# Performance work log

Measured on AMD Instinct MI355X. Metric: run time of the kernel, lower is better.

The kernel has to match this reference:

```python
import jax, jax.numpy as jnp
import numpy as np
from functools import partial

B, T, D = 256, 196, 512
H = 4            # nhead
DH = D // H      # head dim
DFF = 2 * D      # dim_feedforward
K = 8192         # codebook size
L = 2            # num_layers
EPS = 1e-5


def setup_inputs() -> dict:
    key = jax.random.key(0)
    ks = jax.random.split(key, 8)
    s = 0.02  # weight init scale for numerical stability
    return {
        "motion": jax.random.normal(ks[0], (B, T, D), jnp.float32),
        "conv_w": jax.random.normal(ks[1], (L, D, D, 3), jnp.float32) * s,
        "conv_b": jnp.zeros((L, D), jnp.float32),
        "wqkv": jax.random.normal(ks[2], (L, D, 3 * D), jnp.float32) * s,
        "bqkv": jnp.zeros((L, 3 * D), jnp.float32),
        "wo": jax.random.normal(ks[3], (L, D, D), jnp.float32) * s,
        "bo": jnp.zeros((L, D), jnp.float32),
        "ln1_g": jnp.ones((L, D), jnp.float32),
        "ln1_b": jnp.zeros((L, D), jnp.float32),
        "ln2_g": jnp.ones((L, D), jnp.float32),
        "ln2_b": jnp.zeros((L, D), jnp.float32),
        "w1": jax.random.normal(ks[4], (L, D, DFF), jnp.float32) * s,
        "b1": jnp.zeros((L, DFF), jnp.float32),
        "w2": jax.random.normal(ks[5], (L, DFF, D), jnp.float32) * s,
        "b2": jnp.zeros((L, D), jnp.float32),
        "codebook": jax.random.normal(ks[6], (K, D), jnp.float32),
    }


def _layer_norm(x, g, b):
    mu = jnp.mean(x, axis=-1, keepdims=True)
    var = jnp.mean(jnp.square(x - mu), axis=-1, keepdims=True)
    return (x - mu) * jax.lax.rsqrt(var + EPS) * g + b


def _causal_half_downsample(x, w, b):
    # x: [B, T, D] -> [B, ceil(T/2), D]; pad left by repeating first frame (RepeatFirstElementPad1d(2))
    xc = jnp.transpose(x, (0, 2, 1))                       # [B, D, T]
    xp = jnp.concatenate([jnp.repeat(xc[:, :, :1], 2, axis=2), xc], axis=2)
    y = jax.lax.conv_general_dilated(
        xp, w, window_strides=(2,), padding='VALID',
        dimension_numbers=('NCH', 'OIH', 'NCH'))            # [B, D, T//2]
    y = y + b[None, :, None]
    y = jax.nn.gelu(y, approximate=False)                   # torch nn.GELU default = exact
    return jnp.transpose(y, (0, 2, 1))


def _encoder_layer(x, wqkv, bqkv, wo, bo, ln1_g, ln1_b, ln2_g, ln2_b, w1, b1, w2, b2):
    # Post-LN TransformerEncoderLayer with causal self-attention, ReLU FFN (dropout=eval)
    Tl = x.shape[1]
    qkv = x @ wqkv + bqkv                                    # [B, T, 3D]
    q, k, v = jnp.split(qkv, 3, axis=-1)
    q = q.reshape(x.shape[0], Tl, H, DH)
    k = k.reshape(x.shape[0], Tl, H, DH)
    v = v.reshape(x.shape[0], Tl, H, DH)
    scores = jnp.einsum('bqhd,bkhd->bhqk', q, k) / jnp.sqrt(jnp.float32(DH))
    causal = jnp.tril(jnp.ones((Tl, Tl), bool))              # col <= row allowed
    scores = jnp.where(causal[None, None], scores, jnp.float32(-1e30))
    attn = jax.nn.softmax(scores, axis=-1)
    out = jnp.einsum('bhqk,bkhd->bqhd', attn, v).reshape(x.shape[0], Tl, D)
    x = _layer_norm(x + out @ wo + bo, ln1_g, ln1_b)
    ff = jax.nn.relu(x @ w1 + b1) @ w2 + b2
    return _layer_norm(x + ff, ln2_g, ln2_b)


def _quantize(x, codebook):
    # nearest-neighbor VQ with straight-through estimator
    flat = x.reshape(-1, D)                                   # [B*Tf, D]
    d = (jnp.sum(flat * flat, axis=1, keepdims=True)
         - 2.0 * flat @ codebook.T
         + jnp.sum(codebook * codebook, axis=1)[None, :])     # [B*Tf, K]
    idx = jnp.argmin(d, axis=-1)                              # [B*Tf]
    q = codebook[idx]
    q_st = flat + jax.lax.stop_gradient(q - flat)
    return q_st.reshape(x.shape), idx.reshape(x.shape[:2])


def reference(motion, conv_w, conv_b, wqkv, bqkv, wo, bo,
              ln1_g, ln1_b, ln2_g, ln2_b, w1, b1, w2, b2, codebook):
    x = motion
    for l in range(L):  # fixed small layer loop
        x = _causal_half_downsample(x, conv_w[l], conv_b[l])
        x = _encoder_layer(x, wqkv[l], bqkv[l], wo[l], bo[l],
                           ln1_g[l], ln1_b[l], ln2_g[l], ln2_b[l],
                           w1[l], b1[l], w2[l], b2[l])
    quant, idx = _quantize(x, codebook)
    return quant, idx
```

## Files before the change

kernel.cpp:

```cpp
#include <hip/hip_runtime.h>
#include <hip/hip_bf16.h>
#include <math.h>

#define BBATCH 256
#define DMODEL 512
#define NHEAD 4
#define DHEAD 128
#define DFFN 1024
#define KCB 8192
#define VEPS 0.02f
#define NROWS 12544
#define NSPLIT 64

typedef __attribute__((ext_vector_type(8))) short short8v;
typedef __attribute__((ext_vector_type(4))) float f32x4;

__device__ __forceinline__ void tsplit3(float x, unsigned short& h,
                                        unsigned short& m, unsigned short& l) {
    unsigned u = __float_as_uint(x);
    float hf = __uint_as_float(u & 0xffff0000u);
    float r = x - hf;
    unsigned ru = __float_as_uint(r);
    float mf = __uint_as_float(ru & 0xffff0000u);
    float r2 = r - mf;
    h = (unsigned short)(u >> 16);
    m = (unsigned short)(ru >> 16);
    l = (unsigned short)(__float_as_uint(r2) >> 16);
}

__global__ __launch_bounds__(256) void k_wsplit3T(const float* __restrict__ W, int ldw,
                                                  int K, int total,
                                                  unsigned short* __restrict__ th,
                                                  unsigned short* __restrict__ tm,
                                                  unsigned short* __restrict__ tl) {
    int idx = blockIdx.x * 256 + threadIdx.x;
    if (idx >= total) return;
    int n = idx / K, k = idx - n * K;
    unsigned short h, m, l;
    tsplit3(W[(size_t)k * ldw + n], h, m, l);
    th[idx] = h; tm[idx] = m; tl[idx] = l;
}

__global__ __launch_bounds__(256) void k_wsplit3_conv(const float* __restrict__ cw,
                                                      unsigned short* __restrict__ th,
                                                      unsigned short* __restrict__ tm,
                                                      unsigned short* __restrict__ tl) {
    int idx = blockIdx.x * 256 + threadIdx.x;
    if (idx >= DMODEL * 3 * DMODEL) return;
    int dout = idx / 1536, k = idx - dout * 1536;
    int kk = k >> 9, di = k & 511;
    unsigned short h, m, l;
    tsplit3(cw[(size_t)dout * 1536 + di * 3 + kk], h, m, l);
    th[idx] = h; tm[idx] = m; tl[idx] = l;
}

template <int ACT, int CONV>
__global__ __launch_bounds__(256) void k_gemm6(const float* __restrict__ A, int lda,
                                               const unsigned short* __restrict__ B3h,
                                               const unsigned short* __restrict__ B3m,
                                               const unsigned short* __restrict__ B3l,
                                               const float* __restrict__ bias,
                                               float* __restrict__ C, int ldc,
                                               int K, int Tin, int Tout) {
    __shared__ __align__(16) unsigned short Ah[4096], Am[4096], Al[4096];
    __shared__ __align__(16) unsigned short Bh[4096], Bm[4096], Bl[4096];

    int tid = threadIdx.x;
    int lane = tid & 63, wave = tid >> 6;
    int lrow = lane & 15, lkg = lane >> 4;
    int wr = wave >> 1, wc = wave & 1;
    int wrbase = wr * 64, wcbase = wc * 64;
    int n0 = blockIdx.x * 128, m0 = blockIdx.y * 128;

    int sr[2], ss[2]; size_t abase[2], bbase[2]; int attv[2];
#pragma unroll
    for (int rd = 0; rd < 2; rd++) {
        int slot = tid + rd * 256;
        int row = slot >> 2, seg = slot & 3;
        sr[rd] = row; ss[rd] = seg;
        bbase[rd] = (size_t)(n0 + row) * K + seg * 8;
        int m = m0 + row;
        if (CONV) {
            int b = m / Tout, tt = m - b * Tout;
            abase[rd] = (size_t)b * Tin * DMODEL;
            attv[rd] = 2 * tt - 2;
        } else {
            abase[rd] = (size_t)m * lda + seg * 8;
            attv[rd] = 0;
        }
    }

    f32x4 acc[4][4];
#pragma unroll
    for (int mi = 0; mi < 4; mi++)
#pragma unroll
        for (int ni = 0; ni < 4; ni++) acc[mi][ni] = (f32x4){0.0f, 0.0f, 0.0f, 0.0f};

    for (int k0 = 0; k0 < K; k0 += 32) {
#pragma unroll
        for (int rd = 0; rd < 2; rd++) {
            int row = sr[rd], seg = ss[rd];
            int la = row * 32 + ((seg ^ ((row >> 1) & 3)) << 3);
            *(short8v*)(Bh + la) = *(const short8v*)(B3h + bbase[rd] + k0);
            *(short8v*)(Bm + la) = *(const short8v*)(B3m + bbase[rd] + k0);
            *(short8v*)(Bl + la) = *(const short8v*)(B3l + bbase[rd] + k0);
            const float* ap;
            if (CONV) {
                int f = attv[rd] + (k0 >> 9);
                if (f < 0) f = 0;
                ap = A + abase[rd] + (size_t)f * DMODEL + (k0 & 511) + seg * 8;
            } else {
                ap = A + abase[rd] + k0;
            }
            float4 v0 = *(const float4*)ap;
            float4 v1 = *(const float4*)(ap + 4);
            float vv[8] = {v0.x, v0.y, v0.z, v0.w, v1.x, v1.y, v1.z, v1.w};
            short8v hv, mv, lv;
#pragma unroll
            for (int j = 0; j < 8; j++) {
                unsigned short h, m, l;
                tsplit3(vv[j], h, m, l);
                hv[j] = (short)h; mv[j] = (short)m; lv[j] = (short)l;
            }
            *(short8v*)(Ah + la) = hv;
            *(short8v*)(Am + la) = mv;
            *(short8v*)(Al + la) = lv;
        }
        __syncthreads();

        short8v afh[4], afm[4], afl[4];
#pragma unroll
        for (int mi = 0; mi < 4; mi++) {
            int rowa = wrbase + mi * 16 + lrow;
            int off = rowa * 32 + ((lkg ^ ((rowa >> 1) & 3)) << 3);
            afh[mi] = *(const short8v*)(Ah + off);
            afm[mi] = *(const short8v*)(Am + off);
            afl[mi] = *(const short8v*)(Al + off);
        }
#pragma unroll
        for (int ni = 0; ni < 4; ni++) {
            int rowb = wcbase + ni * 16 + lrow;
            int off = rowb * 32 + ((lkg ^ ((rowb >> 1) & 3)) << 3);
            short8v bfh = *(const short8v*)(Bh + off);
            short8v bfm = *(const short8v*)(Bm + off);
            short8v bfl = *(const short8v*)(Bl + off);
#pragma unroll
            for (int mi = 0; mi < 4; mi++) {
                acc[mi][ni] = __builtin_amdgcn_mfma_f32_16x16x32_bf16(afh[mi], bfh, acc[mi][ni], 0, 0, 0);
                acc[mi][ni] = __builtin_amdgcn_mfma_f32_16x16x32_bf16(afh[mi], bfm, acc[mi][ni], 0, 0, 0);
                acc[mi][ni] = __builtin_amdgcn_mfma_f32_16x16x32_bf16(afm[mi], bfh, acc[mi][ni], 0, 0, 0);
                acc[mi][ni] = __builtin_amdgcn_mfma_f32_16x16x32_bf16(afh[mi], bfl, acc[mi][ni], 0, 0, 0);
                acc[mi][ni] = __builtin_amdgcn_mfma_f32_16x16x32_bf16(afl[mi], bfh, acc[mi][ni], 0, 0, 0);
                acc[mi][ni] = __builtin_amdgcn_mfma_f32_16x16x32_bf16(afm[mi], bfm, acc[mi][ni], 0, 0, 0);
            }
        }
        __syncthreads();
    }

    float bv[4];
#pragma unroll
    for (int ni = 0; ni < 4; ni++) bv[ni] = bias[n0 + wcbase + ni * 16 + lrow];
#pragma unroll
    for (int mi = 0; mi < 4; mi++)
#pragma unroll
        for (int ni = 0; ni < 4; ni++)
#pragma unroll
            for (int v = 0; v < 4; v++) {
                int row = m0 + wrbase + mi * 16 + lkg * 4 + v;
                int col = n0 + wcbase + ni * 16 + lrow;
                float x;
                if (ACT == 1) {
                    double dv = (double)acc[mi][ni][v] + (double)bv[ni];
                    dv = 0.5 * dv * (1.0 + erf(dv * 0.7071067811865476));
                    x = (float)dv;
                } else {
                    x = acc[mi][ni][v] + bv[ni];
                    if (ACT == 2) x = x > 0.0f ? x : 0.0f;
                }
                C[(size_t)row * ldc + col] = x;
            }
}

__global__ __launch_bounds__(256) void k_attn(const float* q,
                                              const float* __restrict__ k,
                                              const float* __restrict__ v,
                                              float* out, int T) {
    __shared__ __align__(16) float Ks[98 * 128];
    __shared__ __align__(16) float qsm[4][128];
    __shared__ float psm[4][128];
    int h = blockIdx.x, b = blockIdx.y;
    int tid = threadIdx.x;
    int lane = tid & 63;
    int wave = tid >> 6;
    size_t base = ((size_t)b * T) * DMODEL + (size_t)h * DHEAD;

    float4* Ks4 = (float4*)Ks;
    for (int it = tid; it < T * 32; it += 256) {
        int j = it >> 5, dq = it & 31;
        Ks4[j * 32 + (dq ^ (j & 7))] =
            *(const float4*)&k[base + (size_t)j * DMODEL + dq * 4];
    }
    __syncthreads();

    const float SCALE = 0.08838834764831845f;
    int niter = (T + 3) >> 2;
    for (int i0 = 0; i0 < niter; i0++) {
        int ibase = i0 * 4;
#pragma unroll
        for (int u = 0; u < 2; u++) {
            int idx = tid + u * 256;
            int r = idx >> 7, d = idx & 127;
            int grow = ibase + r;
            if (grow < T) qsm[r][d] = q[base + (size_t)grow * DMODEL + d];
        }
        __syncthreads();

        int i = ibase + wave;
        if (i < T) {
            int j1 = lane;
            int j2 = lane + 64;
            int j2c = j2 < T ? j2 : 0;
            bool a0 = (j1 <= i);
            bool a1 = (j2 <= i);
            const float4* kr1 = Ks4 + j1 * 32;
            const float4* kr2 = Ks4 + j2c * 32;
            const float4* qr = (const float4*)qsm[wave];
            int x1 = j1 & 7, x2 = j2c & 7;
            float4 s0 = {0.f, 0.f, 0.f, 0.f}, s1 = {0.f, 0.f, 0.f, 0.f};
#pragma unroll
            for (int dq = 0; dq < 32; dq++) {
                float4 qv = qr[dq];
                float4 k1 = kr1[dq ^ x1];
                float4 k2 = kr2[dq ^ x2];
                s0.x = fmaf(qv.x, k1.x, s0.x);
                s0.y = fmaf(qv.y, k1.y, s0.y);
                s0.z = fmaf(qv.z, k1.z, s0.z);
                s0.w = fmaf(qv.w, k1.w, s0.w);
                s1.x = fmaf(qv.x, k2.x, s1.x);
                s1.y = fmaf(qv.y, k2.y, s1.y);
                s1.z = fmaf(qv.z, k2.z, s1.z);
                s1.w = fmaf(qv.w, k2.w, s1.w);
            }
            float sv0 = a0 ? ((s0.x + s0.y) + (s0.z + s0.w)) * SCALE : -1e30f;
            float sv1 = a1 ? ((s1.x + s1.y) + (s1.z + s1.w)) * SCALE : -1e30f;

            float m = fmaxf(sv0, sv1);
#pragma unroll
            for (int off = 32; off > 0; off >>= 1) m = fmaxf(m, __shfl_xor(m, off, 64));
            float p0 = a0 ? expf(sv0 - m) : 0.0f;
            float p1 = a1 ? expf(sv1 - m) : 0.0f;
            float sum = p0 + p1;
#pragma unroll
            for (int off = 32; off > 0; off >>= 1) sum += __shfl_xor(sum, off, 64);
            float inv = 1.0f / sum;

            psm[wave][lane] = p0;
            psm[wave][lane + 64] = p1;

            float o0[4] = {0.f, 0.f, 0.f, 0.f}, o1[4] = {0.f, 0.f, 0.f, 0.f};
            const float* vb = v + base;
            for (int j = 0; j <= i; j += 4) {
#pragma unroll
                for (int u = 0; u < 4; u++) {
                    int jj = j + u;
                    float pj = psm[wave][jj];
                    int jr = jj < T ? jj : T - 1;
                    const float* vr = vb + (size_t)jr * DMODEL;
                    o0[u] = fmaf(pj, vr[lane], o0[u]);
                    o1[u] = fmaf(pj, vr[lane + 64], o1[u]);
                }
            }
            out[base + (size_t)i * DMODEL + lane] =
                ((o0[0] + o0[1]) + (o0[2] + o0[3])) * inv;
            out[base + (size_t)i * DMODEL + lane + 64] =
                ((o1[0] + o1[1]) + (o1[2] + o1[3])) * inv;
        }
        __syncthreads();
    }
}

__global__ __launch_bounds__(128) void k_ln(const float* __restrict__ resid,
                                            const float* __restrict__ y,
                                            const float* __restrict__ g,
                                            const float* __restrict__ bta,
                                            float* __restrict__ out) {
    int row = blockIdx.x;
    int tid = threadIdx.x;
    size_t off = (size_t)row * DMODEL;
    double t[4];
#pragma unroll
    for (int i = 0; i < 4; i++) {
        int d = tid + i * 128;
        t[i] = (double)resid[off + d] + (double)y[off + d];
    }
    __shared__ double rd[2];
    double s = t[0] + t[1] + t[2] + t[3];
#pragma unroll
    for (int o = 32; o > 0; o >>= 1) s += __shfl_down(s, o, 64);
    if ((tid & 63) == 0) rd[tid >> 6] = s;
    __syncthreads();
    double mean = (rd[0] + rd[1]) * (1.0 / 512.0);
    double vs = 0.0;
#pragma unroll
    for (int i = 0; i < 4; i++) { double dl = t[i] - mean; vs += dl * dl; }
    __syncthreads();
#pragma unroll
    for (int o = 32; o > 0; o >>= 1) vs += __shfl_down(vs, o, 64);
    if ((tid & 63) == 0) rd[tid >> 6] = vs;
    __syncthreads();
    double var = (rd[0] + rd[1]) * (1.0 / 512.0);
    double scale = 1.0 / sqrt(var + 1e-5);
#pragma unroll
    for (int i = 0; i < 4; i++) {
        int d = tid + i * 128;
        out[off + d] = (float)((t[i] - mean) * scale * (double)g[d] + (double)bta[d]);
    }
}

__global__ __launch_bounds__(64) void k_cbn(const float* __restrict__ cb,
                                            double* __restrict__ cbn) {
    int row = blockIdx.x;
    int tid = threadIdx.x;
    const float* r = cb + (size_t)row * DMODEL;
    double s = 0.0;
    for (int d = tid; d < DMODEL; d += 64) { double v = (double)r[d]; s = fma(v, v, s); }
#pragma unroll
    for (int o = 32; o > 0; o >>= 1) s += __shfl_down(s, o, 64);
    if (tid == 0) cbn[row] = s;
}

__device__ __forceinline__ unsigned short f2bf(float f) {
    unsigned u = __float_as_uint(f);
    unsigned r = (u + 0x7fffu + ((u >> 16) & 1u)) >> 16;
    return (unsigned short)r;
}
__device__ __forceinline__ float bf2f(unsigned short h) {
    return __uint_as_float(((unsigned)h) << 16);
}

__global__ __launch_bounds__(256) void k_split(const float* __restrict__ in,
                                               unsigned short* __restrict__ hi,
                                               unsigned short* __restrict__ lo,
                                               int n4) {
    int i = blockIdx.x * 256 + threadIdx.x;
    if (i >= n4) return;
    float4 v = ((const float4*)in)[i];
    float vv[4] = {v.x, v.y, v.z, v.w};
    unsigned short h[4], l[4];
#pragma unroll
    for (int j = 0; j < 4; j++) {
        h[j] = f2bf(vv[j]);
        l[j] = f2bf(vv[j] - bf2f(h[j]));
    }
    ((ushort4*)hi)[i] = make_ushort4(h[0], h[1], h[2], h[3]);
    ((ushort4*)lo)[i] = make_ushort4(l[0], l[1], l[2], l[3]);
}

__global__ __launch_bounds__(256) void k_cbT(const float* __restrict__ cb,
                                             float* __restrict__ cbT) {
    __shared__ float t[64][65];
    int c0 = blockIdx.x * 64, d0 = blockIdx.y * 64;
    int tid = threadIdx.x;
#pragma unroll
    for (int i = 0; i < 16; i++) {
        int e = tid + i * 256;
        t[e >> 6][e & 63] = cb[(size_t)(c0 + (e >> 6)) * DMODEL + d0 + (e & 63)];
    }
    __syncthreads();
#pragma unroll
    for (int i = 0; i < 16; i++) {
        int e = tid + i * 256;
        int d = e >> 6, c = e & 63;
        cbT[(size_t)(d0 + d) * KCB + c0 + c] = t[c][d];
    }
}

__global__ __launch_bounds__(256) void k_vq1m(const unsigned short* __restrict__ xh,
                                              const unsigned short* __restrict__ xl,
                                              const unsigned short* __restrict__ ch,
                                              const unsigned short* __restrict__ cl,
                                              const double* __restrict__ cbn,
                                              float4* __restrict__ cand) {
    __shared__ __align__(16) unsigned char smem[65536];
    unsigned short* AhU = (unsigned short*)smem;
    unsigned short* AlU = AhU + 8192;
    unsigned short* BhU = AlU + 8192;
    unsigned short* BlU = BhU + 8192;

    int tid = threadIdx.x;
    int lane = tid & 63, wave = tid >> 6;
    int lrow = lane & 15;
    int lkg = lane >> 4;
    int wr = wave >> 1, wc = wave & 1;
    int wrbase = wr * 64, wcbase = wc * 64;

    int wg = (blockIdx.x & 7) * (6272 / 8) + (blockIdx.x >> 3);
    int bx = wg / 98;
    int by = wg % 98;
    int r0 = by * 128, c0 = bx * 128;

    const int srow = tid >> 3;
    const int seg = tid & 7;
    const int sw = seg ^ (srow & 7);

    f32x4 acc[4][4];
#pragma unroll
    for (int m = 0; m < 4; m++)
#pragma unroll
        for (int n = 0; n < 4; n++) acc[m][n] = (f32x4){0.0f, 0.0f, 0.0f, 0.0f};

    for (int ks = 0; ks < 8; ks++) {
        int k0 = ks * 64;
#pragma unroll
        for (int rd = 0; rd < 4; rd++) {
            int row = rd * 32 + srow;
            size_t ga = (((size_t)(r0 + row)) << 9) + k0 + seg * 8;
            size_t gb = (((size_t)(c0 + row)) << 9) + k0 + seg * 8;
            int la = row * 64 + sw * 8;
            *(short8v*)(AhU + la) = *(const short8v*)(xh + ga);
            *(short8v*)(AlU + la) = *(const short8v*)(xl + ga);
            *(short8v*)(BhU + la) = *(const short8v*)(ch + gb);
            *(short8v*)(BlU + la) = *(const short8v*)(cl + gb);
        }
        __syncthreads();
#pragma unroll
        for (int ksub = 0; ksub < 2; ksub++) {
            int segsw = ((ksub * 4 + lkg) ^ (lrow & 7)) * 8;
            short8v afh[4], afl[4], bfh[4], bfl[4];
#pragma unroll
            for (int m = 0; m < 4; m++) {
                int off = (wrbase + m * 16 + lrow) * 64 + segsw;
                afh[m] = *(const short8v*)(AhU + off);
                afl[m] = *(const short8v*)(AlU + off);
            }
#pragma unroll
            for (int n = 0; n < 4; n++) {
                int off = (wcbase + n * 16 + lrow) * 64 + segsw;
                bfh[n] = *(const short8v*)(BhU + off);
                bfl[n] = *(const short8v*)(BlU + off);
            }
#pragma unroll
            for (int m = 0; m < 4; m++)
#pragma unroll
                for (int n = 0; n < 4; n++) {
                    acc[m][n] = __builtin_amdgcn_mfma_f32_16x16x32_bf16(afh[m], bfh[n], acc[m][n], 0, 0, 0);
                    acc[m][n] = __builtin_amdgcn_mfma_f32_16x16x32_bf16(afh[m], bfl[n], acc[m][n], 0, 0, 0);
                    acc[m][n] = __builtin_amdgcn_mfma_f32_16x16x32_bf16(afl[m], bfh[n], acc[m][n], 0, 0, 0);
                }
        }
        __syncthreads();
    }

    float cnv[4];
#pragma unroll
    for (int n = 0; n < 4; n++) cnv[n] = (float)cbn[c0 + wcbase + n * 16 + lrow];

    float* sD = (float*)smem;
    int* sI = (int*)(smem + 32768);
#pragma unroll
    for (int m = 0; m < 4; m++)
#pragma unroll
        for (int v = 0; v < 4; v++) {
            int row = wrbase + m * 16 + lkg * 4 + v;
            float d1 = 1e30f, d2 = 1e30f; int j1 = 0, j2 = 0;
#pragma unroll
            for (int n = 0; n < 4; n++) {
                int code = c0 + wcbase + n * 16 + lrow;
                float d = cnv[n] - 2.0f * acc[m][n][v];
                if (d < d1 || (d == d1 && code < j1)) { d2 = d1; j2 = j1; d1 = d; j1 = code; }
                else if (d < d2 || (d == d2 && code < j2)) { d2 = d; j2 = code; }
            }
            int slot = (wc * 16 + lrow) * 2;
            sD[row * 64 + slot] = d1; sD[row * 64 + slot + 1] = d2;
            sI[row * 64 + slot] = j1; sI[row * 64 + slot + 1] = j2;
        }
    __syncthreads();
    if (tid < 128) {
        float d1 = 1e30f, d2 = 1e30f; int j1 = 0, j2 = 0;
        for (int e = 0; e < 64; e++) {
            float d = sD[tid * 64 + e]; int ix = sI[tid * 64 + e];
            if (d < d1 || (d == d1 && ix < j1)) { d2 = d1; j2 = j1; d1 = d; j1 = ix; }
            else if (d < d2 || (d == d2 && ix < j2)) { d2 = d; j2 = ix; }
        }
        cand[(size_t)bx * NROWS + r0 + tid] =
            make_float4(d1, __int_as_float(j1), d2, __int_as_float(j2));
    }
}

__global__ __launch_bounds__(256) void k_vq2(const float4* __restrict__ cand,
                                             int* __restrict__ idxbuf,
                                             int* __restrict__ flagbuf,
                                             int* __restrict__ flaglist,
                                             int* __restrict__ nflag, int nrows) {
    int row = blockIdx.x * 256 + threadIdx.x;
    if (row >= nrows) return;
    float d1 = 1e30f, d2 = 1e30f; int j1 = 0, j2 = 0;
    for (int s = 0; s < NSPLIT; s++) {
        float4 c = cand[(size_t)s * nrows + row];
        float dd[2] = {c.x, c.z};
        int ii[2] = {__float_as_int(c.y), __float_as_int(c.w)};
#pragma unroll
        for (int e = 0; e < 2; e++) {
            float d = dd[e]; int ix = ii[e];
            if (d < d1 || (d == d1 && ix < j1)) { d2 = d1; j2 = j1; d1 = d; j1 = ix; }
            else if (d < d2 || (d == d2 && ix < j2)) { d2 = d; j2 = ix; }
        }
    }
    idxbuf[row] = j1;
    int f = (d2 - d1 < VEPS) ? 1 : 0;
    flagbuf[row] = f;
    if (f) {
        int pos = atomicAdd(nflag, 1);
        flaglist[pos] = row;
    }
}

__global__ __launch_bounds__(256) void k_vq3a(const float* __restrict__ x,
                                              const float* __restrict__ cbT,
                                              const double* __restrict__ cbn,
                                              const int* __restrict__ flaglist,
                                              const int* __restrict__ nflag,
                                              double* __restrict__ partd,
                                              int* __restrict__ parti) {
    __shared__ __align__(16) float xs[DMODEL];
    __shared__ double sd[256];
    __shared__ int si[256];
    int nf = *nflag;
    int slab = blockIdx.y;
    int tid = threadIdx.x;
    for (int fi = blockIdx.x; fi < nf; fi += gridDim.x) {
        int row = flaglist[fi];
        xs[tid] = x[(size_t)row * DMODEL + tid];
        xs[tid + 256] = x[(size_t)row * DMODEL + tid + 256];
        __syncthreads();
        int c = slab * 256 + tid;
        double a0 = 0.0, a1 = 0.0, a2 = 0.0, a3 = 0.0;
        const float4* xs4 = (const float4*)xs;
#pragma unroll 8
        for (int q = 0; q < DMODEL / 4; q++) {
            float4 xv = xs4[q];
            const float* cp = cbT + (size_t)(q * 4) * KCB + c;
            a0 = fma((double)xv.x, (double)cp[0], a0);
            a1 = fma((double)xv.y, (double)cp[KCB], a1);
            a2 = fma((double)xv.z, (double)cp[2 * KCB], a2);
            a3 = fma((double)xv.w, (double)cp[3 * KCB], a3);
        }
        sd[tid] = cbn[c] - 2.0 * ((a0 + a1) + (a2 + a3));
        si[tid] = c;
        __syncthreads();
        for (int off = 128; off > 0; off >>= 1) {
            if (tid < off) {
                if (sd[tid + off] < sd[tid] ||
                    (sd[tid + off] == sd[tid] && si[tid + off] < si[tid])) {
                    sd[tid] = sd[tid + off]; si[tid] = si[tid + off];
                }
            }
            __syncthreads();
        }
        if (tid == 0) {
            partd[(size_t)row * 32 + slab] = sd[0];
            parti[(size_t)row * 32 + slab] = si[0];
        }
        __syncthreads();
    }
}

__global__ __launch_bounds__(256) void k_vq3b(const float* __restrict__ cb,
                                              const int* __restrict__ idxbuf,
                                              const int* __restrict__ flagbuf,
                                              const double* __restrict__ partd,
                                              const int* __restrict__ parti,
                                              float* __restrict__ outq,
                                              float* __restrict__ outi) {
    int row = blockIdx.x;
    int tid = threadIdx.x;
    __shared__ int bestsh;
    int best = idxbuf[row];
    if (flagbuf[row]) {
        if (tid == 0) {
            double bd = partd[(size_t)row * 32];
            int bi = parti[(size_t)row * 32];
            for (int s = 1; s < 32; s++) {
                double d = partd[(size_t)row * 32 + s];
                int ix = parti[(size_t)row * 32 + s];
                if (d < bd || (d == bd && ix < bi)) { bd = d; bi = ix; }
            }
            bestsh = bi;
        }
        __syncthreads();
        best = bestsh;
    }
    const float* crow = cb + (size_t)best * DMODEL;
    outq[(size_t)row * DMODEL + tid] = crow[tid];
    outq[(size_t)row * DMODEL + tid + 256] = crow[tid + 256];
    if (tid == 0) outi[row] = (float)best;
}

extern "C" void kernel_launch(void* const* d_in, const int* in_sizes, int n_in,
                              void* d_out, int out_size, void* d_ws, size_t ws_size,
                              hipStream_t stream) {
    const float* motion = (const float*)d_in[0];
    const float* conv_w = (const float*)d_in[1];
    const float* conv_b = (const float*)d_in[2];
    const float* wqkv   = (const float*)d_in[3];
    const float* bqkv   = (const float*)d_in[4];
    const float* wo     = (const float*)d_in[5];
    const float* bo     = (const float*)d_in[6];
    const float* ln1g   = (const float*)d_in[7];
    const float* ln1b   = (const float*)d_in[8];
    const float* ln2g   = (const float*)d_in[9];
    const float* ln2b   = (const float*)d_in[10];
    const float* w1     = (const float*)d_in[11];
    const float* b1     = (const float*)d_in[12];
    const float* w2     = (const float*)d_in[13];
    const float* b2     = (const float*)d_in[14];
    const float* cb     = (const float*)d_in[15];

    const size_t SZc = (size_t)25088 * DMODEL;
    float* wsf = (float*)d_ws;
    float*  S0  = wsf + 0 * SZc;
    float*  S1  = wsf + 1 * SZc;
    float*  S2  = wsf + 2 * SZc;
    float*  S3  = wsf + 3 * SZc;
    char* p = (char*)(wsf + 4 * SZc);
    unsigned short* wh = (unsigned short*)p;   p += (size_t)786432 * 2;
    unsigned short* wm = (unsigned short*)p;   p += (size_t)786432 * 2;
    unsigned short* wl = (unsigned short*)p;   p += (size_t)786432 * 2;
    double* cbn    = (double*)p;               p += KCB * 8;
    int*   idxbuf  = (int*)p;                  p += NROWS * 4;
    int*   flagbuf = (int*)p;                  p += NROWS * 4;
    int*   flaglist= (int*)p;                  p += NROWS * 4;
    int*   nflag   = (int*)p;                  p += 256;
    double* partd  = (double*)p;               p += (size_t)NROWS * 32 * 8;
    int*   parti   = (int*)p;                  p += (size_t)NROWS * 32 * 4;

    k_cbn<<<dim3(KCB), dim3(64), 0, stream>>>(cb, cbn);

    const float* xin = motion;
    int Tin = 196;
    for (int l = 0; l < 2; l++) {
        int Tout = Tin / 2;
        int M = BBATCH * Tout;
        const float* wq = wqkv + (size_t)l * DMODEL * 3 * DMODEL;
        const float* bq = bqkv + (size_t)l * 3 * DMODEL;

        k_wsplit3_conv<<<dim3(3072), dim3(256), 0, stream>>>(
            conv_w + (size_t)l * DMODEL * DMODEL * 3, wh, wm, wl);
        k_gemm6<1, 1><<<dim3(4, M / 128), dim3(256), 0, stream>>>(
            xin, DMODEL, wh, wm, wl, conv_b + l * DMODEL, S0, DMODEL,
            3 * DMODEL, Tin, Tout);
        float* qkvdst[3] = {S1, S2, S3};
        for (int s = 0; s < 3; s++) {
            k_wsplit3T<<<dim3(1024), dim3(256), 0, stream>>>(
                wq + s * DMODEL, 3 * DMODEL, DMODEL, DMODEL * DMODEL, wh, wm, wl);
            k_gemm6<0, 0><<<dim3(4, M / 128), dim3(256), 0, stream>>>(
                S0, DMODEL, wh, wm, wl, bq + s * DMODEL, qkvdst[s], DMODEL,
                DMODEL, 1, 1);
        }
        k_attn<<<dim3(NHEAD, BBATCH), dim3(256), 0, stream>>>(S1, S2, S3, S1, Tout);
        k_wsplit3T<<<dim3(1024), dim3(256), 0, stream>>>(
            wo + (size_t)l * DMODEL * DMODEL, DMODEL, DMODEL, DMODEL * DMODEL, wh, wm, wl);
        k_gemm6<0, 0><<<dim3(4, M / 128), dim3(256), 0, stream>>>(
            S1, DMODEL, wh, wm, wl, bo + l * DMODEL, S2, DMODEL, DMODEL, 1, 1);
        k_ln<<<dim3(M), dim3(128), 0, stream>>>(S0, S2, ln1g + l * DMODEL, ln1b + l * DMODEL, S3);
        k_wsplit3T<<<dim3(2048), dim3(256), 0, stream>>>(
            w1 + (size_t)l * DMODEL * DFFN, DFFN, DMODEL, DMODEL * DFFN, wh, wm, wl);
        k_gemm6<2, 0><<<dim3(8, M / 128), dim3(256), 0, stream>>>(
            S3, DMODEL, wh, wm, wl, b1 + l * DFFN, S1, DFFN, DMODEL, 1, 1);
        k_wsplit3T<<<dim3(2048), dim3(256), 0, stream>>>(
            w2 + (size_t)l * DFFN * DMODEL, DMODEL, DFFN, DMODEL * DFFN, wh, wm, wl);
        k_gemm6<0, 0><<<dim3(4, M / 128), dim3(256), 0, stream>>>(
            S1, DFFN, wh, wm, wl, b2 + l * DMODEL, S0, DMODEL, DFFN, 1, 1);
        k_ln<<<dim3(M), dim3(128), 0, stream>>>(S3, S0, ln2g + l * DMODEL, ln2b + l * DMODEL, S1);

        xin = S1;
        Tin = Tout;
    }

    unsigned short* xh = (unsigned short*)S2;
    unsigned short* xl = xh + (size_t)NROWS * DMODEL;
    unsigned short* chb = (unsigned short*)S3;
    unsigned short* clb = chb + (size_t)KCB * DMODEL;
    float4* cand = (float4*)S0;
    k_split<<<dim3(NROWS * DMODEL / 4 / 256), dim3(256), 0, stream>>>(S1, xh, xl,
                                                                      NROWS * DMODEL / 4);
    k_split<<<dim3(KCB * DMODEL / 4 / 256), dim3(256), 0, stream>>>(cb, chb, clb,
                                                                    KCB * DMODEL / 4);

    float* outq = (float*)d_out;
    float* outi = outq + (size_t)NROWS * DMODEL;
    hipMemsetAsync(nflag, 0, sizeof(int), stream);
    k_vq1m<<<dim3(98 * NSPLIT), dim3(256), 0, stream>>>(xh, xl, chb, clb, cbn, cand);
    k_vq2<<<dim3(49), dim3(256), 0, stream>>>(cand, idxbuf, flagbuf, flaglist, nflag, NROWS);
    float* cbT = (float*)S3;
    k_cbT<<<dim3(KCB / 64, DMODEL / 64), dim3(256), 0, stream>>>(cb, cbT);
    k_vq3a<<<dim3(256, 32), dim3(256), 0, stream>>>(S1, cbT, cbn, flaglist, nflag,
                                                    partd, parti);
    k_vq3b<<<dim3(NROWS), dim3(256), 0, stream>>>(cb, idxbuf, flagbuf, partd, parti,
                                                  outq, outi);
}
```

Before: 2.698 ms.

## Tile weight transpose-split, remap GEMM blocks across XCDs, stagger VQ reduce reads

Replaces the strided-read weight split-transpose kernel with a 64x64 shared-memory tiled transpose, so global reads and writes are coalesced. Remaps GEMM workgroup IDs so consecutive tiles land on the same XCD, which is meant to improve L2 reuse of the A/B panels. The VQ candidate reduction staggers its shared-memory index per thread to avoid bank conflicts. The tiled transpose assumes dimensions divisible by 64, and the remap assumes the workgroup count is divisible by 8.

```diff
diff --git a/kernel.cpp b/kernel.cpp
--- a/kernel.cpp
+++ b/kernel.cpp
@@ -28,17 +28,30 @@
     l = (unsigned short)(__float_as_uint(r2) >> 16);
 }
 
-__global__ __launch_bounds__(256) void k_wsplit3T(const float* __restrict__ W, int ldw,
-                                                  int K, int total,
-                                                  unsigned short* __restrict__ th,
-                                                  unsigned short* __restrict__ tm,
-                                                  unsigned short* __restrict__ tl) {
-    int idx = blockIdx.x * 256 + threadIdx.x;
-    if (idx >= total) return;
-    int n = idx / K, k = idx - n * K;
-    unsigned short h, m, l;
-    tsplit3(W[(size_t)k * ldw + n], h, m, l);
-    th[idx] = h; tm[idx] = m; tl[idx] = l;
+__global__ __launch_bounds__(256) void k_wsplit3Tt(const float* __restrict__ W, int ldw,
+                                                   int K,
+                                                   unsigned short* __restrict__ th,
+                                                   unsigned short* __restrict__ tm,
+                                                   unsigned short* __restrict__ tl) {
+    __shared__ float t[64][65];
+    int k0 = blockIdx.x * 64, n0 = blockIdx.y * 64;
+    int tid = threadIdx.x;
+#pragma unroll
+    for (int i = 0; i < 16; i++) {
+        int e = tid + i * 256;
+        int r = e >> 6, c = e & 63;
+        t[r][c] = W[(size_t)(k0 + r) * ldw + n0 + c];
+    }
+    __syncthreads();
+#pragma unroll
+    for (int i = 0; i < 16; i++) {
+        int e = tid + i * 256;
+        int rr = e >> 6, cc = e & 63;
+        unsigned short h, m, l;
+        tsplit3(t[cc][rr], h, m, l);
+        size_t o = (size_t)(n0 + rr) * K + k0 + cc;
+        th[o] = h; tm[o] = m; tl[o] = l;
+    }
 }
 
 __global__ __launch_bounds__(256) void k_wsplit3_conv(const float* __restrict__ cw,
@@ -70,7 +83,12 @@
     int lrow = lane & 15, lkg = lane >> 4;
     int wr = wave >> 1, wc = wave & 1;
     int wrbase = wr * 64, wcbase = wc * 64;
-    int n0 = blockIdx.x * 128, m0 = blockIdx.y * 128;
+
+    int nbx = gridDim.x;
+    int nwg = nbx * gridDim.y;
+    int orig = blockIdx.y * nbx + blockIdx.x;
+    int newid = (orig & 7) * (nwg >> 3) + (orig >> 3);
+    int n0 = (newid % nbx) * 128, m0 = (newid / nbx) * 128;
 
     int sr[2], ss[2]; size_t abase[2], bbase[2]; int attv[2];
 #pragma unroll
@@ -478,7 +496,8 @@
     if (tid < 128) {
         float d1 = 1e30f, d2 = 1e30f; int j1 = 0, j2 = 0;
         for (int e = 0; e < 64; e++) {
-            float d = sD[tid * 64 + e]; int ix = sI[tid * 64 + e];
+            int s = (e + tid) & 63;
+            float d = sD[tid * 64 + s]; int ix = sI[tid * 64 + s];
             if (d < d1 || (d == d1 && ix < j1)) { d2 = d1; j2 = j1; d1 = d; j1 = ix; }
             else if (d < d2 || (d == d2 && ix < j2)) { d2 = d; j2 = ix; }
         }
@@ -651,24 +670,24 @@
             3 * DMODEL, Tin, Tout);
         float* qkvdst[3] = {S1, S2, S3};
         for (int s = 0; s < 3; s++) {
-            k_wsplit3T<<<dim3(1024), dim3(256), 0, stream>>>(
-                wq + s * DMODEL, 3 * DMODEL, DMODEL, DMODEL * DMODEL, wh, wm, wl);
+            k_wsplit3Tt<<<dim3(8, 8), dim3(256), 0, stream>>>(
+                wq + s * DMODEL, 3 * DMODEL, DMODEL, wh, wm, wl);
             k_gemm6<0, 0><<<dim3(4, M / 128), dim3(256), 0, stream>>>(
                 S0, DMODEL, wh, wm, wl, bq + s * DMODEL, qkvdst[s], DMODEL,
                 DMODEL, 1, 1);
         }
         k_attn<<<dim3(NHEAD, BBATCH), dim3(256), 0, stream>>>(S1, S2, S3, S1, Tout);
-        k_wsplit3T<<<dim3(1024), dim3(256), 0, stream>>>(
-            wo + (size_t)l * DMODEL * DMODEL, DMODEL, DMODEL, DMODEL * DMODEL, wh, wm, wl);
+        k_wsplit3Tt<<<dim3(8, 8), dim3(256), 0, stream>>>(
+            wo + (size_t)l * DMODEL * DMODEL, DMODEL, DMODEL, wh, wm, wl);
         k_gemm6<0, 0><<<dim3(4, M / 128), dim3(256), 0, stream>>>(
             S1, DMODEL, wh, wm, wl, bo + l * DMODEL, S2, DMODEL, DMODEL, 1, 1);
         k_ln<<<dim3(M), dim3(128), 0, stream>>>(S0, S2, ln1g + l * DMODEL, ln1b + l * DMODEL, S3);
-        k_wsplit3T<<<dim3(2048), dim3(256), 0, stream>>>(
-            w1 + (size_t)l * DMODEL * DFFN, DFFN, DMODEL, DMODEL * DFFN, wh, wm, wl);
+        k_wsplit3Tt<<<dim3(8, 16), dim3(256), 0, stream>>>(
+            w1 + (size_t)l * DMODEL * DFFN, DFFN, DMODEL, wh, wm, wl);
         k_gemm6<2, 0><<<dim3(8, M / 128), dim3(256), 0, stream>>>(
             S3, DMODEL, wh, wm, wl, b1 + l * DFFN, S1, DFFN, DMODEL, 1, 1);
-        k_wsplit3T<<<dim3(2048), dim3(256), 0, stream>>>(
-            w2 + (size_t)l * DFFN * DMODEL, DMODEL, DFFN, DMODEL * DFFN, wh, wm, wl);
+        k_wsplit3Tt<<<dim3(16, 8), dim3(256), 0, stream>>>(
+            w2 + (size_t)l * DFFN * DMODEL, DMODEL, DFFN, wh, wm, wl);
         k_gemm6<0, 0><<<dim3(4, M / 128), dim3(256), 0, stream>>>(
             S1, DFFN, wh, wm, wl, b2 + l * DMODEL, S0, DMODEL, DFFN, 1, 1);
         k_ln<<<dim3(M), dim3(128), 0, stream>>>(S3, S0, ln2g + l * DMODEL, ln2b + l * DMODEL, S1);
```

After: 2.559 ms. -5.2%, faster.
